# Performance work log

Measured on AMD Instinct MI355X. Metric: run time of the kernel, lower is better.

The kernel has to match this reference:

```python
import jax, jax.numpy as jnp
import numpy as np

TEMPERATURE = 0.1

def _l2norm(x):
    # F.normalize(dim=1) with eps clamp
    n = jnp.maximum(jnp.linalg.norm(x, axis=1, keepdims=True), 1e-12)
    return x / n

def _retrieval_metric(s):
    # T=1: position of the diagonal element in each row's descending sort.
    order = jnp.argsort(-s, axis=1)            # [N,N] descending argsort
    rankpos = jnp.argsort(order, axis=1)        # inverse permutation: rank of each column
    pos = jnp.diagonal(rankpos)                 # j such that rank[i][j] == i
    posf = pos.astype(s.dtype)
    r1 = jnp.mean((pos < 1).astype(s.dtype))
    r5 = jnp.mean((pos < 5).astype(s.dtype))
    r10 = jnp.mean((pos < 10).astype(s.dtype))
    mr = jnp.mean(posf)
    return r1, r5, r10, mr

def setup_inputs() -> dict:
    key = jax.random.key(0)
    k1, k2, k3, k4 = jax.random.split(key, 4)
    N, C = 4096, 512
    return {
        'v_feat': jax.random.normal(k1, (N, C), dtype=jnp.float32),
        't_feat': jax.random.normal(k2, (N, C), dtype=jnp.float32),
        'p_v': jax.random.normal(k3, (N, C), dtype=jnp.float32),
        'p_t': jax.random.normal(k4, (N, C), dtype=jnp.float32),
    }

def reference(v_feat, t_feat, p_v, p_t):
    vn = _l2norm(v_feat)
    tn = _l2norm(t_feat)
    pvn = _l2norm(p_v)
    ptn = _l2norm(p_t)
    sv = jnp.einsum('nc,mc->nm', vn, ptn) / TEMPERATURE  # [N,N]
    st = jnp.einsum('nc,mc->nm', tn, pvn) / TEMPERATURE  # [N,N]
    # nominator: scalar logsumexp over both diagonals (2N values)
    nominator = jax.nn.logsumexp(jnp.concatenate([jnp.diagonal(sv), jnp.diagonal(st)], axis=0))
    # denominator: per-row logsumexp over concatenated [N,2N]
    denominator = jax.nn.logsumexp(jnp.concatenate([sv, st], axis=1), axis=1)
    loss = jnp.mean(denominator - nominator)
    # metrics (no-grad path in original)
    v_std = jnp.mean(jnp.std(vn, axis=0, ddof=1))
    t_std = jnp.mean(jnp.std(tn, axis=0, ddof=1))
    pv_std = jnp.mean(jnp.std(pvn, axis=0, ddof=1))
    pt_std = jnp.mean(jnp.std(ptn, axis=0, ddof=1))
    sv_raw = jnp.einsum('nc,mc->nm', vn, ptn)
    st_raw = jnp.einsum('nc,mc->nm', tn, pvn)
    v_r1, v_r5, v_r10, v_mr = _retrieval_metric(sv_raw)
    t_r1, t_r5, t_r10, t_mr = _retrieval_metric(st_raw)
    return (loss, v_std, t_std, pv_std, pt_std,
            v_r1, v_r5, v_r10, v_mr,
            t_r1, t_r5, t_r10, t_mr)
```

## Files before the change

kernel.cpp:

```cpp
#include <hip/hip_runtime.h>
#include <hip/hip_bf16.h>

#define N 4096
#define C 512

typedef __attribute__((ext_vector_type(8))) short bf16x8;
typedef __attribute__((ext_vector_type(8))) short s16x8;
typedef __attribute__((ext_vector_type(4))) float f32x4;

__device__ inline float bf2f(__hip_bfloat16 h) { return __bfloat162float(h); }
__device__ inline float bfbits2f(unsigned short b) {
    union { unsigned u; float f; } c; c.u = ((unsigned)b) << 16; return c.f;
}

__device__ inline void gload16(const void* g, void* l) {
    __builtin_amdgcn_global_load_lds(
        (__attribute__((address_space(1))) void*)(g),
        (__attribute__((address_space(3))) void*)(l),
        16, 0, 0);
}

__global__ __launch_bounds__(256) void k_prep(
    const float* __restrict__ s0, const float* __restrict__ s1f,
    const float* __restrict__ s2f, const float* __restrict__ s3,
    __hip_bfloat16* __restrict__ ws_hi0, long mat_stride,
    float* __restrict__ dv, float* __restrict__ dt,
    float* __restrict__ st1, float* __restrict__ st2,
    unsigned int* __restrict__ counter)
{
    __shared__ float sa[4][512];
    __shared__ float sb[4][512];

    const int b = blockIdx.x;
    const int tid = threadIdx.x;
    const int lane = tid & 63;
    const int w = tid >> 6;

    if (b == 0 && tid == 0) *counter = 0;

    if (b < 4096) {
        const int grow = b * 4 + w;
        const int m = grow >> 12;
        const int row = grow & 4095;
        const float* src = (m == 0) ? s0 : (m == 1) ? s1f : (m == 2) ? s2f : s3;
        __hip_bfloat16* hi = ws_hi0 + (long)m * mat_stride;
        __hip_bfloat16* lo = hi + (long)N * C;

        const float4* r4 = (const float4*)(src + (size_t)row * C);
        float4 x0 = r4[lane * 2];
        float4 x1 = r4[lane * 2 + 1];
        float ss = x0.x*x0.x + x0.y*x0.y + x0.z*x0.z + x0.w*x0.w
                 + x1.x*x1.x + x1.y*x1.y + x1.z*x1.z + x1.w*x1.w;
        for (int o = 1; o < 64; o <<= 1) ss += __shfl_xor(ss, o);
        float scale = 1.0f / fmaxf(sqrtf(ss), 1e-12f);
        float y[8] = { x0.x*scale, x0.y*scale, x0.z*scale, x0.w*scale,
                       x1.x*scale, x1.y*scale, x1.z*scale, x1.w*scale };
        __hip_bfloat16 hv[8], lv[8];
        for (int e = 0; e < 8; e++) {
            hv[e] = __float2bfloat16(y[e]);
            lv[e] = __float2bfloat16(y[e] - bf2f(hv[e]));
        }
        size_t base = (size_t)row * C + lane * 8;
        *(s16x8*)(hi + base) = *(s16x8*)hv;
        *(s16x8*)(lo + base) = *(s16x8*)lv;
    } else if (b < 6144) {
        const int idx = b - 4096;
        const int z = idx >> 10;
        const int row = (idx & 1023) * 4 + w;
        const float* A = z ? s1f : s0;
        const float* B = z ? s2f : s3;
        float* dout = z ? dt : dv;

        const float4* a4 = (const float4*)(A + (size_t)row * C);
        const float4* b4 = (const float4*)(B + (size_t)row * C);
        float4 a0 = a4[lane * 2], a1 = a4[lane * 2 + 1];
        float4 b0 = b4[lane * 2], b1 = b4[lane * 2 + 1];
        float ssa = a0.x*a0.x + a0.y*a0.y + a0.z*a0.z + a0.w*a0.w
                  + a1.x*a1.x + a1.y*a1.y + a1.z*a1.z + a1.w*a1.w;
        float ssb = b0.x*b0.x + b0.y*b0.y + b0.z*b0.z + b0.w*b0.w
                  + b1.x*b1.x + b1.y*b1.y + b1.z*b1.z + b1.w*b1.w;
        float dot = a0.x*b0.x + a0.y*b0.y + a0.z*b0.z + a0.w*b0.w
                  + a1.x*b1.x + a1.y*b1.y + a1.z*b1.z + a1.w*b1.w;
        for (int o = 1; o < 64; o <<= 1) {
            ssa += __shfl_xor(ssa, o);
            ssb += __shfl_xor(ssb, o);
            dot += __shfl_xor(dot, o);
        }
        if (lane == 0)
            dout[row] = dot / (fmaxf(sqrtf(ssa), 1e-12f) * fmaxf(sqrtf(ssb), 1e-12f));
    } else {
        const int idx = b - 6144;
        const int m = idx >> 5;
        const int chunk = idx & 31;
        const float* src = (m == 0) ? s0 : (m == 1) ? s1f : (m == 2) ? s2f : s3;
        const int slice = w;

        float a[8], q[8];
        for (int e = 0; e < 8; e++) { a[e] = 0.f; q[e] = 0.f; }
        const int row0 = chunk * 128 + slice * 32;
        for (int r = 0; r < 32; r++) {
            const float4* r4 = (const float4*)(src + (size_t)(row0 + r) * C);
            float4 x0 = r4[lane * 2];
            float4 x1 = r4[lane * 2 + 1];
            float ss = x0.x*x0.x + x0.y*x0.y + x0.z*x0.z + x0.w*x0.w
                     + x1.x*x1.x + x1.y*x1.y + x1.z*x1.z + x1.w*x1.w;
            for (int o = 1; o < 64; o <<= 1) ss += __shfl_xor(ss, o);
            float scale = 1.0f / fmaxf(sqrtf(ss), 1e-12f);
            float y[8] = { x0.x*scale, x0.y*scale, x0.z*scale, x0.w*scale,
                           x1.x*scale, x1.y*scale, x1.z*scale, x1.w*scale };
            for (int e = 0; e < 8; e++) { a[e] += y[e]; q[e] += y[e] * y[e]; }
        }
        for (int e = 0; e < 8; e++) {
            sa[slice][lane * 8 + e] = a[e];
            sb[slice][lane * 8 + e] = q[e];
        }
        __syncthreads();
        for (int c = tid; c < 512; c += 256) {
            float A = sa[0][c] + sa[1][c] + sa[2][c] + sa[3][c];
            float B = sb[0][c] + sb[1][c] + sb[2][c] + sb[3][c];
            size_t o = ((size_t)m * 32 + chunk) * 512 + c;
            st1[o] = A;
            st2[o] = B;
        }
    }
}

__global__ __launch_bounds__(256) void k_gemm(
    const __hip_bfloat16* __restrict__ h0, const __hip_bfloat16* __restrict__ l0,
    const __hip_bfloat16* __restrict__ h1, const __hip_bfloat16* __restrict__ l1,
    const __hip_bfloat16* __restrict__ h2, const __hip_bfloat16* __restrict__ l2,
    const __hip_bfloat16* __restrict__ h3, const __hip_bfloat16* __restrict__ l3,
    const float* __restrict__ dv, const float* __restrict__ dt,
    float* __restrict__ pev, float* __restrict__ pet,
    float* __restrict__ pcv, float* __restrict__ pct)
{
    __shared__ __align__(16) __hip_bfloat16 sA[2][128][32];
    __shared__ __align__(16) __hip_bfloat16 sB[2][128][32];
    __shared__ float sdiag[128];
    __shared__ float sred[128][2][2];

    const int z = blockIdx.z;
    const __hip_bfloat16* Ah = z ? h1 : h0;
    const __hip_bfloat16* Al = z ? l1 : l0;
    const __hip_bfloat16* Bh = z ? h2 : h3;
    const __hip_bfloat16* Bl = z ? l2 : l3;
    const float* diag = z ? dt : dv;
    float* pe = z ? pet : pev;
    float* pc = z ? pct : pcv;

    const int tid = threadIdx.x;
    const int lane = tid & 63;
    const int w = tid >> 6;
    const int wy = w >> 1, wx = w & 1;
    const int bm = blockIdx.x * 128;
    const int bn = blockIdx.y * 128;

    if (tid < 128) sdiag[tid] = diag[bm + tid];

    f32x4 acc[4][4];
    for (int i = 0; i < 4; i++)
        for (int j = 0; j < 4; j++)
            acc[i][j] = (f32x4){0.f, 0.f, 0.f, 0.f};

    const int srow = lane >> 2;
    const int lcol = (lane & 3) * 8;
    const int scolg = (((lane & 3) ^ ((lane >> 3) & 3))) * 8;
    const int fr = lane & 15;
    const int pcs = ((lane >> 4) ^ ((fr >> 1) & 3)) * 8;

    for (int k0 = 0; k0 < C; k0 += 32) {
        for (int half = 0; half < 2; half++) {
            int rr = w * 16 + half * 64 + srow;
            size_t ga = (size_t)(bm + rr) * C + k0 + scolg;
            size_t gb = (size_t)(bn + rr) * C + k0 + scolg;
            gload16(Ah + ga, &sA[0][rr][lcol]);
            gload16(Al + ga, &sA[1][rr][lcol]);
            gload16(Bh + gb, &sB[0][rr][lcol]);
            gload16(Bl + gb, &sB[1][rr][lcol]);
        }
        __syncthreads();

        bf16x8 a_h[4], a_l[4], b_h[4], b_l[4];
        for (int i = 0; i < 4; i++) {
            a_h[i] = *(const bf16x8*)&sA[0][wy * 64 + i * 16 + fr][pcs];
            a_l[i] = *(const bf16x8*)&sA[1][wy * 64 + i * 16 + fr][pcs];
            b_h[i] = *(const bf16x8*)&sB[0][wx * 64 + i * 16 + fr][pcs];
            b_l[i] = *(const bf16x8*)&sB[1][wx * 64 + i * 16 + fr][pcs];
        }
        for (int i = 0; i < 4; i++)
            for (int j = 0; j < 4; j++) {
                acc[i][j] = __builtin_amdgcn_mfma_f32_16x16x32_bf16(a_h[i], b_h[j], acc[i][j], 0, 0, 0);
                acc[i][j] = __builtin_amdgcn_mfma_f32_16x16x32_bf16(a_h[i], b_l[j], acc[i][j], 0, 0, 0);
                acc[i][j] = __builtin_amdgcn_mfma_f32_16x16x32_bf16(a_l[i], b_h[j], acc[i][j], 0, 0, 0);
            }
        __syncthreads();
    }

    const int quad = lane >> 4;
    for (int i = 0; i < 4; i++) {
        for (int reg = 0; reg < 4; reg++) {
            int rloc = wy * 64 + i * 16 + quad * 4 + reg;
            int grow = bm + rloc;
            float d = sdiag[rloc];
            float e = 0.f, c = 0.f;
            for (int j = 0; j < 4; j++) {
                float s = acc[i][j][reg];
                int gcol = bn + wx * 64 + j * 16 + fr;
                e += __expf(10.f * s - 10.f);
                if (s > d && gcol != grow) c += 1.f;
            }
            for (int o = 1; o < 16; o <<= 1) {
                e += __shfl_xor(e, o);
                c += __shfl_xor(c, o);
            }
            if (fr == 0) { sred[rloc][wx][0] = e; sred[rloc][wx][1] = c; }
        }
    }
    __syncthreads();
    if (tid < 128) {
        size_t idx = (size_t)(bm + tid) * 32 + blockIdx.y;
        pe[idx] = sred[tid][0][0] + sred[tid][1][0];
        pc[idx] = sred[tid][0][1] + sred[tid][1][1];
    }
}

__global__ __launch_bounds__(64) void k_fin(
    const float* __restrict__ dv, const float* __restrict__ dt,
    const float* __restrict__ pev, const float* __restrict__ pet,
    const float* __restrict__ pcv, const float* __restrict__ pct,
    const float* __restrict__ st1, const float* __restrict__ st2,
    float* __restrict__ partials, float* __restrict__ stdpart,
    unsigned int* __restrict__ counter, float* __restrict__ out)
{
    const int b = blockIdx.x;
    const int lane = threadIdx.x;

    if (b < 64) {
        const int row = b * 64 + lane;
        float se = 0.f, pv = 0.f, pt = 0.f;
        const float4* e4v = (const float4*)(pev + (size_t)row * 32);
        const float4* e4t = (const float4*)(pet + (size_t)row * 32);
        const float4* c4v = (const float4*)(pcv + (size_t)row * 32);
        const float4* c4t = (const float4*)(pct + (size_t)row * 32);
        for (int q = 0; q < 8; q++) {
            float4 a = e4v[q], bb = e4t[q], c = c4v[q], d = c4t[q];
            se += a.x + a.y + a.z + a.w + bb.x + bb.y + bb.z + bb.w;
            pv += c.x + c.y + c.z + c.w;
            pt += d.x + d.y + d.z + d.w;
        }
        float vals[10];
        vals[0] = logf(se) + 10.f;
        vals[1] = (pv < 0.5f) ? 1.f : 0.f;
        vals[2] = (pv < 4.5f) ? 1.f : 0.f;
        vals[3] = (pv < 9.5f) ? 1.f : 0.f;
        vals[4] = pv;
        vals[5] = (pt < 0.5f) ? 1.f : 0.f;
        vals[6] = (pt < 4.5f) ? 1.f : 0.f;
        vals[7] = (pt < 9.5f) ? 1.f : 0.f;
        vals[8] = pt;
        vals[9] = __expf(10.f * dv[row] - 10.f) + __expf(10.f * dt[row] - 10.f);
        for (int k = 0; k < 10; k++) {
            float v = vals[k];
            for (int o = 1; o < 64; o <<= 1) v += __shfl_xor(v, o);
            if (lane == k) partials[(size_t)b * 10 + k] = v;
        }
    } else {
        const int idx = b - 64;
        const int m = idx >> 3;
        const int col = (idx & 7) * 64 + lane;
        float a = 0.f, q = 0.f;
        for (int ch = 0; ch < 32; ch++) {
            size_t o = ((size_t)m * 32 + ch) * 512 + col;
            a += st1[o];
            q += st2[o];
        }
        float var = (q - a * a * (1.f / N)) * (1.f / (N - 1));
        float sd = sqrtf(fmaxf(var, 0.f));
        for (int o = 1; o < 64; o <<= 1) sd += __shfl_xor(sd, o);
        if (lane == 0) stdpart[idx] = sd;
    }

    __syncthreads();
    __shared__ unsigned int s_old;
    if (lane == 0) {
        __threadfence();
        s_old = atomicAdd(counter, 1u);
    }
    __syncthreads();
    if (s_old != 95) return;
    __threadfence();

    float v = 0.f;
    if (lane < 10) {
        for (int k = 0; k < 64; k++) v += partials[k * 10 + lane];
    }
    __shared__ float g[10];
    __shared__ float stds[4];
    if (lane < 10) g[lane] = v;
    if (lane < 4) {
        float s = 0.f;
        for (int i = 0; i < 8; i++) s += stdpart[lane * 8 + i];
        stds[lane] = s * (1.f / 512.f);
    }
    __syncthreads();
    if (lane == 0) {
        const float invN = 1.f / N;
        float nominator = logf(g[9]) + 10.f;
        out[0]  = g[0] * invN - nominator;
        out[1]  = stds[0];
        out[2]  = stds[1];
        out[3]  = stds[2];
        out[4]  = stds[3];
        out[5]  = g[1] * invN;
        out[6]  = g[2] * invN;
        out[7]  = g[3] * invN;
        out[8]  = g[4] * invN;
        out[9]  = g[5] * invN;
        out[10] = g[6] * invN;
        out[11] = g[7] * invN;
        out[12] = g[8] * invN;
    }
}

extern "C" void kernel_launch(void* const* d_in, const int* in_sizes, int n_in,
                              void* d_out, int out_size, void* d_ws, size_t ws_size,
                              hipStream_t stream)
{
    char* p = (char*)d_ws;
    const size_t NE = (size_t)N * C;
    const long mat_stride = 2 * NE;
    __hip_bfloat16* hiA[4];
    __hip_bfloat16* loA[4];
    for (int m = 0; m < 4; m++) {
        hiA[m] = (__hip_bfloat16*)p; p += NE * 2;
        loA[m] = (__hip_bfloat16*)p; p += NE * 2;
    }
    float* dv  = (float*)p; p += N * 4;
    float* dt  = (float*)p; p += N * 4;
    float* pev = (float*)p; p += 32 * N * 4;
    float* pet = (float*)p; p += 32 * N * 4;
    float* pcv = (float*)p; p += 32 * N * 4;
    float* pct = (float*)p; p += 32 * N * 4;
    float* st1 = (float*)p; p += 4 * 32 * 512 * 4;
    float* st2 = (float*)p; p += 4 * 32 * 512 * 4;
    float* partials = (float*)p; p += 64 * 10 * 4;
    float* stdpart  = (float*)p; p += 32 * 4;
    unsigned int* counter = (unsigned int*)p; p += 16;

    k_prep<<<dim3(6272), 256, 0, stream>>>(
        (const float*)d_in[0], (const float*)d_in[1],
        (const float*)d_in[2], (const float*)d_in[3],
        hiA[0], mat_stride, dv, dt, st1, st2, counter);

    k_gemm<<<dim3(32, 32, 2), 256, 0, stream>>>(
        hiA[0], loA[0], hiA[1], loA[1], hiA[2], loA[2], hiA[3], loA[3],
        dv, dt, pev, pet, pcv, pct);

    k_fin<<<dim3(96), 64, 0, stream>>>(
        dv, dt, pev, pet, pcv, pct, st1, st2,
        partials, stdpart, counter, (float*)d_out);
}
```

Baseline: 217.0 us.

## Fuse normalize, diagonal dot and column-stat passes in prep kernel

Merges the three separate block roles of the prep kernel (bf16 hi/lo split, diagonal cosine, per-column sum and sum-of-squares) into one pass where each block handles 16 rows of one matrix. Each input row is read from global memory once instead of up to three times, and only the second matrix of each pair is re-read for the diagonal. Partial column statistics grow from 32 to 256 chunks per matrix, so the finalize kernel must sum eight times more partials per column.

```diff
diff --git a/kernel.cpp b/kernel.cpp
--- a/kernel.cpp
+++ b/kernel.cpp
@@ -9,9 +9,6 @@
 typedef __attribute__((ext_vector_type(4))) float f32x4;
 
 __device__ inline float bf2f(__hip_bfloat16 h) { return __bfloat162float(h); }
-__device__ inline float bfbits2f(unsigned short b) {
-    union { unsigned u; float f; } c; c.u = ((unsigned)b) << 16; return c.f;
-}
 
 __device__ inline void gload16(const void* g, void* l) {
     __builtin_amdgcn_global_load_lds(
@@ -29,7 +26,7 @@
     unsigned int* __restrict__ counter)
 {
     __shared__ float sa[4][512];
-    __shared__ float sb[4][512];
+    __shared__ float sq[4][512];
 
     const int b = blockIdx.x;
     const int tid = threadIdx.x;
@@ -38,14 +35,20 @@
 
     if (b == 0 && tid == 0) *counter = 0;
 
-    if (b < 4096) {
-        const int grow = b * 4 + w;
-        const int m = grow >> 12;
-        const int row = grow & 4095;
-        const float* src = (m == 0) ? s0 : (m == 1) ? s1f : (m == 2) ? s2f : s3;
-        __hip_bfloat16* hi = ws_hi0 + (long)m * mat_stride;
-        __hip_bfloat16* lo = hi + (long)N * C;
-
+    const int m = b >> 8;
+    const int chunk = b & 255;
+    const float* src = (m == 0) ? s0 : (m == 1) ? s1f : (m == 2) ? s2f : s3;
+    const float* srcB = (m == 0) ? s3 : s2f;
+    float* dout = (m == 0) ? dv : dt;
+    __hip_bfloat16* hi = ws_hi0 + (long)m * mat_stride;
+    __hip_bfloat16* lo = hi + (long)N * C;
+
+    float a[8], q[8];
+    for (int e = 0; e < 8; e++) { a[e] = 0.f; q[e] = 0.f; }
+
+    const int row0 = chunk * 16 + w * 4;
+    for (int i = 0; i < 4; i++) {
+        const int row = row0 + i;
         const float4* r4 = (const float4*)(src + (size_t)row * C);
         float4 x0 = r4[lane * 2];
         float4 x1 = r4[lane * 2 + 1];
@@ -53,75 +56,47 @@
                  + x1.x*x1.x + x1.y*x1.y + x1.z*x1.z + x1.w*x1.w;
         for (int o = 1; o < 64; o <<= 1) ss += __shfl_xor(ss, o);
         float scale = 1.0f / fmaxf(sqrtf(ss), 1e-12f);
+
         float y[8] = { x0.x*scale, x0.y*scale, x0.z*scale, x0.w*scale,
                        x1.x*scale, x1.y*scale, x1.z*scale, x1.w*scale };
         __hip_bfloat16 hv[8], lv[8];
         for (int e = 0; e < 8; e++) {
             hv[e] = __float2bfloat16(y[e]);
             lv[e] = __float2bfloat16(y[e] - bf2f(hv[e]));
+            a[e] += y[e];
+            q[e] += y[e] * y[e];
         }
         size_t base = (size_t)row * C + lane * 8;
         *(s16x8*)(hi + base) = *(s16x8*)hv;
         *(s16x8*)(lo + base) = *(s16x8*)lv;
-    } else if (b < 6144) {
-        const int idx = b - 4096;
-        const int z = idx >> 10;
-        const int row = (idx & 1023) * 4 + w;
-        const float* A = z ? s1f : s0;
-        const float* B = z ? s2f : s3;
-        float* dout = z ? dt : dv;
-
-        const float4* a4 = (const float4*)(A + (size_t)row * C);
-        const float4* b4 = (const float4*)(B + (size_t)row * C);
-        float4 a0 = a4[lane * 2], a1 = a4[lane * 2 + 1];
-        float4 b0 = b4[lane * 2], b1 = b4[lane * 2 + 1];
-        float ssa = a0.x*a0.x + a0.y*a0.y + a0.z*a0.z + a0.w*a0.w
-                  + a1.x*a1.x + a1.y*a1.y + a1.z*a1.z + a1.w*a1.w;
-        float ssb = b0.x*b0.x + b0.y*b0.y + b0.z*b0.z + b0.w*b0.w
-                  + b1.x*b1.x + b1.y*b1.y + b1.z*b1.z + b1.w*b1.w;
-        float dot = a0.x*b0.x + a0.y*b0.y + a0.z*b0.z + a0.w*b0.w
-                  + a1.x*b1.x + a1.y*b1.y + a1.z*b1.z + a1.w*b1.w;
-        for (int o = 1; o < 64; o <<= 1) {
-            ssa += __shfl_xor(ssa, o);
-            ssb += __shfl_xor(ssb, o);
-            dot += __shfl_xor(dot, o);
-        }
-        if (lane == 0)
-            dout[row] = dot / (fmaxf(sqrtf(ssa), 1e-12f) * fmaxf(sqrtf(ssb), 1e-12f));
-    } else {
-        const int idx = b - 6144;
-        const int m = idx >> 5;
-        const int chunk = idx & 31;
-        const float* src = (m == 0) ? s0 : (m == 1) ? s1f : (m == 2) ? s2f : s3;
-        const int slice = w;
-
-        float a[8], q[8];
-        for (int e = 0; e < 8; e++) { a[e] = 0.f; q[e] = 0.f; }
-        const int row0 = chunk * 128 + slice * 32;
-        for (int r = 0; r < 32; r++) {
-            const float4* r4 = (const float4*)(src + (size_t)(row0 + r) * C);
-            float4 x0 = r4[lane * 2];
-            float4 x1 = r4[lane * 2 + 1];
-            float ss = x0.x*x0.x + x0.y*x0.y + x0.z*x0.z + x0.w*x0.w
-                     + x1.x*x1.x + x1.y*x1.y + x1.z*x1.z + x1.w*x1.w;
-            for (int o = 1; o < 64; o <<= 1) ss += __shfl_xor(ss, o);
-            float scale = 1.0f / fmaxf(sqrtf(ss), 1e-12f);
-            float y[8] = { x0.x*scale, x0.y*scale, x0.z*scale, x0.w*scale,
-                           x1.x*scale, x1.y*scale, x1.z*scale, x1.w*scale };
-            for (int e = 0; e < 8; e++) { a[e] += y[e]; q[e] += y[e] * y[e]; }
-        }
-        for (int e = 0; e < 8; e++) {
-            sa[slice][lane * 8 + e] = a[e];
-            sb[slice][lane * 8 + e] = q[e];
-        }
-        __syncthreads();
-        for (int c = tid; c < 512; c += 256) {
-            float A = sa[0][c] + sa[1][c] + sa[2][c] + sa[3][c];
-            float B = sb[0][c] + sb[1][c] + sb[2][c] + sb[3][c];
-            size_t o = ((size_t)m * 32 + chunk) * 512 + c;
-            st1[o] = A;
-            st2[o] = B;
-        }
+
+        if (m < 2) {
+            const float4* b4 = (const float4*)(srcB + (size_t)row * C);
+            float4 b0 = b4[lane * 2], b1 = b4[lane * 2 + 1];
+            float ssb = b0.x*b0.x + b0.y*b0.y + b0.z*b0.z + b0.w*b0.w
+                      + b1.x*b1.x + b1.y*b1.y + b1.z*b1.z + b1.w*b1.w;
+            float dot = x0.x*b0.x + x0.y*b0.y + x0.z*b0.z + x0.w*b0.w
+                      + x1.x*b1.x + x1.y*b1.y + x1.z*b1.z + x1.w*b1.w;
+            for (int o = 1; o < 64; o <<= 1) {
+                ssb += __shfl_xor(ssb, o);
+                dot += __shfl_xor(dot, o);
+            }
+            if (lane == 0)
+                dout[row] = dot * scale / fmaxf(sqrtf(ssb), 1e-12f);
+        }
+    }
+
+    for (int e = 0; e < 8; e++) {
+        sa[w][lane * 8 + e] = a[e];
+        sq[w][lane * 8 + e] = q[e];
+    }
+    __syncthreads();
+    for (int c = tid; c < 512; c += 256) {
+        float A = sa[0][c] + sa[1][c] + sa[2][c] + sa[3][c];
+        float B = sq[0][c] + sq[1][c] + sq[2][c] + sq[3][c];
+        size_t o = ((size_t)m * 256 + chunk) * 512 + c;
+        st1[o] = A;
+        st2[o] = B;
     }
 }
 
@@ -242,11 +217,11 @@
         const float4* e4t = (const float4*)(pet + (size_t)row * 32);
         const float4* c4v = (const float4*)(pcv + (size_t)row * 32);
         const float4* c4t = (const float4*)(pct + (size_t)row * 32);
-        for (int q = 0; q < 8; q++) {
-            float4 a = e4v[q], bb = e4t[q], c = c4v[q], d = c4t[q];
-            se += a.x + a.y + a.z + a.w + bb.x + bb.y + bb.z + bb.w;
-            pv += c.x + c.y + c.z + c.w;
-            pt += d.x + d.y + d.z + d.w;
+        for (int qd = 0; qd < 8; qd++) {
+            float4 aa = e4v[qd], bb = e4t[qd], cc = c4v[qd], dd = c4t[qd];
+            se += aa.x + aa.y + aa.z + aa.w + bb.x + bb.y + bb.z + bb.w;
+            pv += cc.x + cc.y + cc.z + cc.w;
+            pt += dd.x + dd.y + dd.z + dd.w;
         }
         float vals[10];
         vals[0] = logf(se) + 10.f;
@@ -269,8 +244,8 @@
         const int m = idx >> 3;
         const int col = (idx & 7) * 64 + lane;
         float a = 0.f, q = 0.f;
-        for (int ch = 0; ch < 32; ch++) {
-            size_t o = ((size_t)m * 32 + ch) * 512 + col;
+        for (int ch = 0; ch < 256; ch++) {
+            size_t o = ((size_t)m * 256 + ch) * 512 + col;
             a += st1[o];
             q += st2[o];
         }
@@ -341,13 +316,13 @@
     float* pet = (float*)p; p += 32 * N * 4;
     float* pcv = (float*)p; p += 32 * N * 4;
     float* pct = (float*)p; p += 32 * N * 4;
-    float* st1 = (float*)p; p += 4 * 32 * 512 * 4;
-    float* st2 = (float*)p; p += 4 * 32 * 512 * 4;
+    float* st1 = (float*)p; p += 4 * 256 * 512 * 4;
+    float* st2 = (float*)p; p += 4 * 256 * 512 * 4;
     float* partials = (float*)p; p += 64 * 10 * 4;
     float* stdpart  = (float*)p; p += 32 * 4;
     unsigned int* counter = (unsigned int*)p; p += 16;
 
-    k_prep<<<dim3(6272), 256, 0, stream>>>(
+    k_prep<<<dim3(1024), 256, 0, stream>>>(
         (const float*)d_in[0], (const float*)d_in[1],
         (const float*)d_in[2], (const float*)d_in[3],
         hiA[0], mat_stride, dv, dt, st1, st2, counter);
```

Result: no change. 214.0 us (-1.4%).
